# Kernel optimization log

Measured on AMD Instinct MI355X. Metric: run time of the kernel, lower is better.

The kernel has to match this reference:

```python
import jax, jax.numpy as jnp
import numpy as np

B, T, Rn, D, O, E, H, C, TM = 20, 20, 20, 4096, 16, 512, 8, 68, 1900


def l2norm(x, axis=-1, eps=1e-12):
    return x / jnp.maximum(jnp.linalg.norm(x, axis=axis, keepdims=True), eps)


def setup_inputs() -> dict:
    key = jax.random.key(0)
    ks = jax.random.split(key, 10)
    return {
        "features": jax.random.normal(ks[0], (B, T, Rn, D), jnp.float32),
        "labels": jax.random.randint(ks[1], (B, O), 0, C),
        "temporal_mem": jax.random.normal(ks[2], (TM, T, D), jnp.float32),
        "entity_W": jax.random.normal(ks[3], (C, E), jnp.float32) / np.float32(np.sqrt(C)),
        "entity_b": jnp.zeros((E,), jnp.float32),
        "Wq": jax.random.normal(ks[4], (E, E), jnp.float32) / np.float32(np.sqrt(E)),
        "Wk": jax.random.normal(ks[5], (D, E), jnp.float32) / np.float32(np.sqrt(D)),
        "Wv": jax.random.normal(ks[6], (D, E), jnp.float32) / np.float32(np.sqrt(D)),
        "Wo": jax.random.normal(ks[7], (E, E), jnp.float32) / np.float32(np.sqrt(E)),
        "obj_W1": jax.random.normal(ks[8], (D, E), jnp.float32) / np.float32(np.sqrt(D)),
        "obj_b1": jnp.zeros((E,), jnp.float32),
        "obj_W2": jax.random.normal(ks[9], (E, 1), jnp.float32) / np.float32(np.sqrt(E)),
        "obj_b2": jnp.zeros((1,), jnp.float32),
    }


def reference(features, labels, temporal_mem, entity_W, entity_b, Wq, Wk, Wv, Wo,
              obj_W1, obj_b1, obj_W2, obj_b2):
    beta = 0.5   # loss mixing weight (module's beta)
    qgce = 0.7   # generalized-CE exponent
    Dh = E // H
    # region features, L2-normalized (dataset_feat == 'CVPR' path)
    Rf = l2norm(features)                                   # [B,T,Rn,D]

    # ---- temporal memory-bank kNN retrieval ----
    R_max = l2norm(jnp.max(Rf, axis=2))                     # [B,T,D] max-pool over regions
    mem_max = l2norm(jnp.max(temporal_mem, axis=1))         # [TM,D] max-pool over frames
    sim = jnp.einsum('btd,md->btm', R_max, mem_max)         # [B,T,TM]
    idx = jnp.argmax(sim, axis=-1)                          # [B,T] nearest memory slot
    Rp = temporal_mem[idx]                                  # [B,T,T,D] gathered memory videos
    mem_feat = jnp.max(Rp, axis=2)                          # [B,T,D]

    # ---- entity (object-label) embedding: one-hot with class 0 zeroed ----
    onehot = jax.nn.one_hot(labels, C, dtype=features.dtype)
    onehot = onehot * (labels != 0)[..., None].astype(features.dtype)
    Qe = onehot @ entity_W + entity_b                       # [B,O,E]

    # ---- multi-head attention fusion over regions + retrieved memory ----
    kv = jnp.concatenate([Rf.reshape(B, T * Rn, D), mem_feat], axis=1)  # [B,N,D]
    q = (Qe @ Wq).reshape(B, O, H, Dh)
    k = (kv @ Wk).reshape(B, -1, H, Dh)
    v = (kv @ Wv).reshape(B, -1, H, Dh)
    scores = jnp.einsum('bohd,bnhd->bhon', q, k) / np.float32(np.sqrt(Dh))
    attn = jax.nn.softmax(scores, axis=-1)
    fused = jnp.einsum('bhon,bnhd->bohd', attn, v).reshape(B, O, E) @ Wo  # [B,O,E]

    # ---- top-k region objectness selection + generalized CE ----
    QR = jax.lax.stop_gradient(jnp.mean(scores, axis=1)[:, :, :T * Rn].reshape(B, O, T, Rn))
    hi = jnp.argmax(QR, axis=-1)                            # [B,O,T] top-1 region
    lo = jnp.argmin(QR, axis=-1)                            # [B,O,T] low region
    bidx = jnp.arange(B)[:, None, None]
    tidx = jnp.arange(T)[None, None, :]
    R_high = Rf[bidx, tidx, hi]                             # [B,O,T,D]
    R_low = Rf[bidx, tidx, lo]                              # [B,O,T,D]
    osel = (labels != 0).astype(features.dtype)             # [B,O]
    onum = jnp.maximum(jnp.sum(osel, axis=1), 1.0)
    mlp = lambda x: jax.nn.sigmoid(jnp.tanh(x @ obj_W1 + obj_b1) @ obj_W2 + obj_b2)
    s_hi = mlp(R_high * osel[..., None, None]).squeeze(-1)  # [B,O,T]
    s_lo = mlp(R_low * osel[..., None, None]).squeeze(-1)
    gce_hi = jnp.mean((1.0 - (s_hi + 1e-7) ** qgce) / qgce * osel[..., None], axis=-1)
    gce_lo = jnp.mean((1.0 - (1.0 - s_lo + 1e-7) ** qgce) / qgce * osel[..., None], axis=-1)
    gce = jnp.mean(jnp.sum(gce_hi, axis=1) / onum) + jnp.mean(jnp.sum(gce_lo, axis=1) / onum)

    return fused + beta * gce
```

## Files before the change

kernel.cpp:

```cpp
#include <hip/hip_runtime.h>

#define B_   20
#define T_   20
#define RN   20
#define D_   4096
#define O_   16
#define E_   512
#define H_   8
#define DH   64
#define TM_  1900
#define MREG 8192
#define NW   1536
#define NSIM 2048
#define MSIM 512
#define NG   1024
#define CAP  256
#define SIMK 8
#define GK   4

using f32x4  = __attribute__((ext_vector_type(4))) float;
using bf16x8 = __attribute__((ext_vector_type(8))) __bf16;

__device__ __forceinline__ unsigned short f2bf(float f){
  unsigned u = __float_as_uint(f);
  u += 0x7fffu + ((u >> 16) & 1u);
  return (unsigned short)(u >> 16);
}

__device__ __forceinline__ void st_bf4(unsigned short* dst, float4 v){
  ushort4 o = make_ushort4(f2bf(v.x), f2bf(v.y), f2bf(v.z), f2bf(v.w));
  *(ushort4*)dst = o;
}

__device__ __forceinline__ float bsum256(float v, float* sh){
  int t = threadIdx.x;
  for (int o = 32; o; o >>= 1) v += __shfl_down(v, o, 64);
  __syncthreads();
  if ((t & 63) == 0) sh[t >> 6] = v;
  __syncthreads();
  return sh[0] + sh[1] + sh[2] + sh[3];
}

__device__ __forceinline__ float bmax256(float v, float* sh){
  int t = threadIdx.x;
  for (int o = 32; o; o >>= 1) v = fmaxf(v, __shfl_down(v, o, 64));
  __syncthreads();
  if ((t & 63) == 0) sh[t >> 6] = v;
  __syncthreads();
  return fmaxf(fmaxf(sh[0], sh[1]), fmaxf(sh[2], sh[3]));
}

__device__ __forceinline__ void gld16(const void* g, void* l){
  __builtin_amdgcn_global_load_lds(
      (const __attribute__((address_space(1))) unsigned int*)g,
      (__attribute__((address_space(3))) unsigned int*)l, 16, 0, 0);
}

__global__ __launch_bounds__(256) void k_prelight(
    const float* __restrict__ F,
    const float* __restrict__ Wk, const float* __restrict__ Wv, const float* __restrict__ W1,
    unsigned short* __restrict__ Wall,
    unsigned short* __restrict__ A, float* __restrict__ rmaxr, float* __restrict__ rmsum,
    unsigned short* __restrict__ ubf,
    const int* __restrict__ labels, const float* __restrict__ entW, const float* __restrict__ entB,
    const float* __restrict__ Wq, float* __restrict__ q){
  __shared__ char smem[4352];
  int bid = blockIdx.x, t = threadIdx.x;
  if (bid < 512){
    int bt = bid;
    if (bt >= 400){
      int4 zz = make_int4(0,0,0,0);
      int4* r1 = (int4*)(ubf + (size_t)bt*D_);
      r1[t] = zz; r1[t + 256] = zz;
      int base = 8000 + (bt - 400)*2;
#pragma unroll
      for (int k = 0; k < 2; ++k){
        if (base + k < MREG){
          int4* r2 = (int4*)(A + (size_t)(base + k)*D_);
          r2[t] = zz; r2[t + 256] = zz;
        }
      }
      return;
    }
    float* sh = (float*)smem;
    const float* fb = F + (size_t)bt*RN*D_;
    unsigned short* ab = A + (size_t)bt*RN*D_;
    float4 mx[4];
#pragma unroll
    for (int i = 0; i < 4; ++i) mx[i] = make_float4(-1e30f,-1e30f,-1e30f,-1e30f);
    float4 vn[4];
#pragma unroll
    for (int i = 0; i < 4; ++i) vn[i] = *(const float4*)(fb + i*1024 + t*4);
    for (int r = 0; r < RN; ++r){
      float4 v[4];
      float s = 0.f;
#pragma unroll
      for (int i = 0; i < 4; ++i){
        v[i] = vn[i];
        s += v[i].x*v[i].x + v[i].y*v[i].y + v[i].z*v[i].z + v[i].w*v[i].w;
      }
      if (r + 1 < RN){
#pragma unroll
        for (int i = 0; i < 4; ++i)
          vn[i] = *(const float4*)(fb + (size_t)(r+1)*D_ + i*1024 + t*4);
      }
      s = bsum256(s, sh);
      float ri = 1.f / fmaxf(sqrtf(s), 1e-12f);
#pragma unroll
      for (int i = 0; i < 4; ++i){
        v[i].x *= ri; v[i].y *= ri; v[i].z *= ri; v[i].w *= ri;
        st_bf4(ab + (size_t)r*D_ + i*1024 + t*4, v[i]);
        mx[i].x = fmaxf(mx[i].x, v[i].x); mx[i].y = fmaxf(mx[i].y, v[i].y);
        mx[i].z = fmaxf(mx[i].z, v[i].z); mx[i].w = fmaxf(mx[i].w, v[i].w);
      }
    }
    float s2 = 0.f;
#pragma unroll
    for (int i = 0; i < 4; ++i){
      *(float4*)(rmaxr + (size_t)bt*D_ + i*1024 + t*4) = mx[i];
      s2 += mx[i].x*mx[i].x + mx[i].y*mx[i].y + mx[i].z*mx[i].z + mx[i].w*mx[i].w;
    }
    s2 = bsum256(s2, sh);
    if (t == 0) rmsum[bt] = s2;
    float inv = 1.f / fmaxf(sqrtf(s2), 1e-12f);
#pragma unroll
    for (int i = 0; i < 4; ++i){
      float4 u = mx[i];
      u.x *= inv; u.y *= inv; u.z *= inv; u.w *= inv;
      st_bf4(ubf + (size_t)bt*D_ + i*1024 + t*4, u);
    }
  } else if (bid < 6656){
    int wti = bid - 512;
    float* tile = (float*)smem;
    int kb = (wti & 127) * 32, nb = (wti >> 7) * 32;
    const float* src; int nc0;
    if (nb < 512)      { src = Wk; nc0 = nb; }
    else if (nb < 1024){ src = Wv; nc0 = nb - 512; }
    else               { src = W1; nc0 = nb - 1024; }
    int tx = t & 31, ty = t >> 5;
#pragma unroll
    for (int j = 0; j < 4; ++j){
      int k = kb + ty + j*8;
      tile[(ty + j*8)*33 + tx] = src[(size_t)k*E_ + nc0 + tx];
    }
    __syncthreads();
#pragma unroll
    for (int j = 0; j < 4; ++j){
      int n = nb + ty + j*8;
      int k = kb + tx;
      Wall[(size_t)n*D_ + k] = f2bf(tile[tx*33 + ty + j*8]);
    }
  } else {
    int bo = bid - 6656;
    float* qe = (float*)smem;
    int lab = labels[bo];
    float sel = (lab != 0) ? 1.f : 0.f;
    qe[t]       = sel * entW[(size_t)lab*E_ + t]       + entB[t];
    qe[t + 256] = sel * entW[(size_t)lab*E_ + t + 256] + entB[t + 256];
    __syncthreads();
    float a0 = 0.f, a1 = 0.f;
    for (int ep = 0; ep < E_; ++ep){
      float r = qe[ep];
      a0 += r * Wq[(size_t)ep*E_ + t];
      a1 += r * Wq[(size_t)ep*E_ + t + 256];
    }
    q[(size_t)bo*E_ + t] = a0;
    q[(size_t)bo*E_ + t + 256] = a1;
  }
}

__global__ __launch_bounds__(512, 1) void k_mix(
    const unsigned short* __restrict__ Akv, const unsigned short* __restrict__ Wall,
    float* __restrict__ C2,
    const float* __restrict__ TMm, float* __restrict__ umax, float* __restrict__ msum,
    unsigned short* __restrict__ gbf){
  __shared__ char lds[131072];
  int bid = blockIdx.x, t = threadIdx.x;
  if (bid < 192){
    int sb = (bid & 7)*24 + (bid >> 3);
    int mt = sb / 6, nt = sb % 6;
    int tid = t, wid = tid >> 6, l = tid & 63;
    int wr = (wid >> 2) * 128;
    int wc = (wid & 3) * 64;
    int fr = l & 15, fq = l >> 4;
    const char* Ab = (const char*)Akv + (size_t)mt*256*(size_t)(D_*2);
    const char* Bb = (const char*)Wall + (size_t)nt*256*(size_t)(D_*2);
    f32x4 acc[8][4];
#pragma unroll
    for (int m = 0; m < 8; ++m)
#pragma unroll
      for (int n = 0; n < 4; ++n) acc[m][n] = (f32x4){0.f,0.f,0.f,0.f};
#pragma unroll
    for (int i = 0; i < 4; ++i){
      int idx = i*512 + tid;
      int row = idx >> 3, u = idx & 7;
      int ul = u ^ (row & 7);
      gld16(Ab + (size_t)row*(D_*2) + (size_t)(ul*16), lds + idx*16);
      gld16(Bb + (size_t)row*(D_*2) + (size_t)(ul*16), lds + 32768 + idx*16);
    }
    __syncthreads();
    int c = 0;
    for (int kt = 0; kt < D_/64; ++kt){
      if (kt < D_/64 - 1){
        int ktoff = (kt + 1) * 128;
        char* dA = lds + (c^1)*65536;
        char* dB = dA + 32768;
#pragma unroll
        for (int i = 0; i < 4; ++i){
          int idx = i*512 + tid;
          int row = idx >> 3, u = idx & 7;
          int ul = u ^ (row & 7);
          gld16(Ab + (size_t)row*(D_*2) + ktoff + ul*16, dA + idx*16);
          gld16(Bb + (size_t)row*(D_*2) + ktoff + ul*16, dB + idx*16);
        }
      }
      const char* LA = lds + c*65536;
      const char* LB = LA + 32768;
      bf16x8 bv[4][2];
#pragma unroll
      for (int n = 0; n < 4; ++n)
#pragma unroll
        for (int kk = 0; kk < 2; ++kk){
          int row = wc + n*16 + fr;
          int u = (kk*4 + fq) ^ (row & 7);
          bv[n][kk] = *(const bf16x8*)(LB + row*128 + u*16);
        }
      __builtin_amdgcn_s_setprio(1);
#pragma unroll
      for (int mp = 0; mp < 4; ++mp){
        bf16x8 av[2][2];
#pragma unroll
        for (int mm = 0; mm < 2; ++mm)
#pragma unroll
          for (int kk = 0; kk < 2; ++kk){
            int row = wr + (mp*2 + mm)*16 + fr;
            int u = (kk*4 + fq) ^ (row & 7);
            av[mm][kk] = *(const bf16x8*)(LA + row*128 + u*16);
          }
#pragma unroll
        for (int mm = 0; mm < 2; ++mm)
#pragma unroll
          for (int n = 0; n < 4; ++n)
#pragma unroll
            for (int kk = 0; kk < 2; ++kk)
              acc[mp*2 + mm][n] = __builtin_amdgcn_mfma_f32_16x16x32_bf16(
                  av[mm][kk], bv[n][kk], acc[mp*2 + mm][n], 0, 0, 0);
      }
      __builtin_amdgcn_s_setprio(0);
      __syncthreads();
      c ^= 1;
    }
    size_t crow0 = (size_t)mt*256 + wr, ccol0 = (size_t)nt*256 + wc;
#pragma unroll
    for (int m = 0; m < 8; ++m)
#pragma unroll
      for (int n = 0; n < 4; ++n){
        size_t r0 = crow0 + m*16 + fq*4, c0 = ccol0 + n*16 + fr;
#pragma unroll
        for (int j = 0; j < 4; ++j)
          C2[(r0 + j)*(size_t)NW + c0] = acc[m][n][j];
      }
  } else {
    int m = bid - 192;
    if (m >= TM_){
      int4 zz = make_int4(0,0,0,0);
      ((int4*)(gbf + (size_t)m*D_))[t] = zz;
      return;
    }
    float* sh = (float*)lds;
    const float* base = TMm + (size_t)m*T_*D_;
    float4 mx[2];
#pragma unroll
    for (int i = 0; i < 2; ++i) mx[i] = make_float4(-1e30f,-1e30f,-1e30f,-1e30f);
    float4 va[2][2];
#pragma unroll
    for (int i = 0; i < 2; ++i) va[0][i] = *(const float4*)(base + i*2048 + t*4);
#pragma unroll
    for (int f = 0; f < T_; ++f){
      int c = f & 1;
      if (f + 1 < T_){
#pragma unroll
        for (int i = 0; i < 2; ++i)
          va[c^1][i] = *(const float4*)(base + (size_t)(f+1)*D_ + i*2048 + t*4);
      }
#pragma unroll
      for (int i = 0; i < 2; ++i){
        mx[i].x = fmaxf(mx[i].x, va[c][i].x); mx[i].y = fmaxf(mx[i].y, va[c][i].y);
        mx[i].z = fmaxf(mx[i].z, va[c][i].z); mx[i].w = fmaxf(mx[i].w, va[c][i].w);
      }
    }
    float s = 0.f;
#pragma unroll
    for (int i = 0; i < 2; ++i){
      *(float4*)(umax + (size_t)m*D_ + i*2048 + t*4) = mx[i];
      st_bf4(gbf + (size_t)m*D_ + i*2048 + t*4, mx[i]);
      s += mx[i].x*mx[i].x + mx[i].y*mx[i].y + mx[i].z*mx[i].z + mx[i].w*mx[i].w;
    }
    for (int o = 32; o; o >>= 1) s += __shfl_down(s, o, 64);
    __syncthreads();
    if ((t & 63) == 0) sh[t >> 6] = s;
    __syncthreads();
    if (t == 0){
      float tot = 0.f;
#pragma unroll
      for (int w = 0; w < 8; ++w) tot += sh[w];
      msum[m] = tot;
    }
  }
}

__global__ __launch_bounds__(512, 1) void k_simg(
    const unsigned short* __restrict__ ubf, const unsigned short* __restrict__ gbf,
    const unsigned short* __restrict__ Wall,
    float* __restrict__ simp, float* __restrict__ Gcp){
  __shared__ char lds[131072];
  int bid = blockIdx.x;
  bid = (bid & 7)*32 + (bid >> 3);
  const unsigned short *A, *Bw; float* C; int ldc, mt, nt, kt0, nkt;
  if (bid < 128){
    int p = bid >> 4, s = bid & 15;
    A = ubf; Bw = gbf; C = simp + (size_t)p*MSIM*NSIM; ldc = NSIM;
    mt = s >> 3; nt = s & 7; kt0 = p*(64/SIMK); nkt = 64/SIMK;
  } else {
    int s2 = bid - 128;
    int p = s2 >> 5, idx = s2 & 31;
    A = gbf; Bw = Wall; C = Gcp + (size_t)p*NSIM*NG; ldc = NG;
    mt = idx >> 2; nt = idx & 3; kt0 = p*(64/GK); nkt = 64/GK;
  }
  int tid = threadIdx.x, wid = tid >> 6, l = tid & 63;
  int wr = (wid >> 2) * 128;
  int wc = (wid & 3) * 64;
  int fr = l & 15, fq = l >> 4;
  const char* Ab = (const char*)A + (size_t)mt*256*(size_t)(D_*2);
  const char* Bb = (const char*)Bw + (size_t)nt*256*(size_t)(D_*2);
  f32x4 acc[8][4];
#pragma unroll
  for (int m = 0; m < 8; ++m)
#pragma unroll
    for (int n = 0; n < 4; ++n) acc[m][n] = (f32x4){0.f,0.f,0.f,0.f};
#pragma unroll
  for (int i = 0; i < 4; ++i){
    int idx = i*512 + tid;
    int row = idx >> 3, u = idx & 7;
    int ul = u ^ (row & 7);
    gld16(Ab + (size_t)row*(D_*2) + (size_t)(kt0*128 + ul*16), lds + idx*16);
    gld16(Bb + (size_t)row*(D_*2) + (size_t)(kt0*128 + ul*16), lds + 32768 + idx*16);
  }
  __syncthreads();
  int c = 0;
  for (int kt = kt0; kt < kt0 + nkt; ++kt){
    if (kt < kt0 + nkt - 1){
      int ktoff = (kt + 1) * 128;
      char* dA = lds + (c^1)*65536;
      char* dB = dA + 32768;
#pragma unroll
      for (int i = 0; i < 4; ++i){
        int idx = i*512 + tid;
        int row = idx >> 3, u = idx & 7;
        int ul = u ^ (row & 7);
        gld16(Ab + (size_t)row*(D_*2) + ktoff + ul*16, dA + idx*16);
        gld16(Bb + (size_t)row*(D_*2) + ktoff + ul*16, dB + idx*16);
      }
    }
    const char* LA = lds + c*65536;
    const char* LB = LA + 32768;
    bf16x8 bv[4][2];
#pragma unroll
    for (int n = 0; n < 4; ++n)
#pragma unroll
      for (int kk = 0; kk < 2; ++kk){
        int row = wc + n*16 + fr;
        int u = (kk*4 + fq) ^ (row & 7);
        bv[n][kk] = *(const bf16x8*)(LB + row*128 + u*16);
      }
    __builtin_amdgcn_s_setprio(1);
#pragma unroll
    for (int mp = 0; mp < 4; ++mp){
      bf16x8 av[2][2];
#pragma unroll
      for (int mm = 0; mm < 2; ++mm)
#pragma unroll
        for (int kk = 0; kk < 2; ++kk){
          int row = wr + (mp*2 + mm)*16 + fr;
          int u = (kk*4 + fq) ^ (row & 7);
          av[mm][kk] = *(const bf16x8*)(LA + row*128 + u*16);
        }
#pragma unroll
      for (int mm = 0; mm < 2; ++mm)
#pragma unroll
        for (int n = 0; n < 4; ++n)
#pragma unroll
          for (int kk = 0; kk < 2; ++kk)
            acc[mp*2 + mm][n] = __builtin_amdgcn_mfma_f32_16x16x32_bf16(
                av[mm][kk], bv[n][kk], acc[mp*2 + mm][n], 0, 0, 0);
    }
    __builtin_amdgcn_s_setprio(0);
    __syncthreads();
    c ^= 1;
  }
  size_t crow0 = (size_t)mt*256 + wr, ccol0 = (size_t)nt*256 + wc;
#pragma unroll
  for (int m = 0; m < 8; ++m)
#pragma unroll
    for (int n = 0; n < 4; ++n){
      size_t r0 = crow0 + m*16 + fq*4, c0 = ccol0 + n*16 + fr;
#pragma unroll
      for (int j = 0; j < 4; ++j)
        C[(r0 + j)*(size_t)ldc + c0] = acc[m][n][j];
    }
}

__global__ __launch_bounds__(256) void k_pick(const float* __restrict__ simp,
                                              const float* __restrict__ rmaxr, const float* __restrict__ rmsum,
                                              const float* __restrict__ umax, const float* __restrict__ msum,
                                              const float* __restrict__ Gcp, float* __restrict__ C2){
  int bt = blockIdx.x, t = threadIdx.x;
  __shared__ float srow[1920];
  __shared__ float sh[4];
  __shared__ int cnt;
  __shared__ int cl[CAP];
  for (int m = t; m < TM_; m += 256){
    float s = 0.f;
#pragma unroll
    for (int p = 0; p < SIMK; ++p)
      s += simp[(size_t)p*MSIM*NSIM + (size_t)bt*NSIM + m];
    srow[m] = s * (1.f / fmaxf(sqrtf(msum[m]), 1e-12f));
  }
  if (t == 0) cnt = 0;
  __syncthreads();
  float mx = -1e30f;
  for (int m = t; m < TM_; m += 256) mx = fmaxf(mx, srow[m]);
  mx = bmax256(mx, sh);
  float thr = mx - 2.5e-4f;
  for (int m = t; m < TM_; m += 256){
    if (srow[m] >= thr){
      int p = atomicAdd(&cnt, 1);
      if (p < CAP) cl[p] = m;
    }
  }
  __syncthreads();
  int cn = cnt < CAP ? cnt : CAP;
  float rinvv = 1.f / fmaxf(sqrtf(rmsum[bt]), 1e-12f);
  const float* a = rmaxr + (size_t)bt*D_;
  float best = -1e30f; int bestm = 0x7fffffff;
  for (int ci = 0; ci < cn; ++ci){
    int m = cl[ci];
    const float* wrow = umax + (size_t)m*D_;
    float p = 0.f;
    for (int i = t*4; i < D_; i += 1024){
      float4 av = *(const float4*)(a + i);
      float4 wv = *(const float4*)(wrow + i);
      p += av.x*wv.x + av.y*wv.y + av.z*wv.z + av.w*wv.w;
    }
    p = bsum256(p, sh);
    float sim = p * rinvv * (1.f / fmaxf(sqrtf(msum[m]), 1e-12f));
    if (sim > best || (sim == best && m < bestm)){ best = sim; bestm = m; }
  }
  float* dst = C2 + (size_t)(MREG + bt)*NW;
  int j = t*4;
  float4 accv = make_float4(0.f,0.f,0.f,0.f);
#pragma unroll
  for (int p = 0; p < GK; ++p){
    float4 v = *(const float4*)(Gcp + (size_t)p*NSIM*NG + (size_t)bestm*NG + j);
    accv.x += v.x; accv.y += v.y; accv.z += v.z; accv.w += v.w;
  }
  *(float4*)(dst + j) = accv;
}

__global__ __launch_bounds__(256) void k_post(const float* __restrict__ q, const float* __restrict__ c2,
                                              float* __restrict__ fpre, int* __restrict__ hi,
                                              int* __restrict__ lo, const float* __restrict__ b1,
                                              const float* __restrict__ W2, const float* __restrict__ b2,
                                              float* __restrict__ z){
  __shared__ char smem[58368];
  int bid = blockIdx.x, t = threadIdx.x;
  if (bid < 160){
    int b = bid >> 3, h = bid & 7;
    int w = t >> 6, l = t & 63;
    float* qhp = (float*)smem;
    float* kb  = (float*)(smem + 4160);
    float* sc  = (float*)(smem + 31460);
    for (int i = t; i < O_*DH; i += 256){
      int o = i >> 6, d = i & 63;
      qhp[o*65 + d] = q[((size_t)(b*O_ + o))*E_ + h*DH + d] * 0.125f;
    }
    __syncthreads();
    for (int c = 0; c < 4; ++c){
      for (int i = t; i < 105*DH; i += 256){
        int j = i >> 6, d = i & 63;
        int n = c*105 + j;
        size_t row = n < 400 ? (size_t)b*400 + n : (size_t)MREG + b*20 + (n - 400);
        kb[j*65 + d] = c2[row*NW + h*DH + d];
      }
      __syncthreads();
      for (int i = t; i < O_*105; i += 256){
        int o = i / 105, j = i % 105;
        float acc = 0.f;
        for (int d = 0; d < DH; ++d) acc += qhp[o*65 + d] * kb[j*65 + d];
        sc[o*420 + c*105 + j] = acc;
      }
      __syncthreads();
    }
    for (int oi = 0; oi < 4; ++oi){
      int o = w + oi*4;
      float mxv = -1e30f;
      for (int n = l; n < 420; n += 64) mxv = fmaxf(mxv, sc[o*420 + n]);
      for (int of = 32; of; of >>= 1) mxv = fmaxf(mxv, __shfl_xor(mxv, of, 64));
      float sum = 0.f;
      for (int n = l; n < 420; n += 64){ float e = expf(sc[o*420 + n] - mxv); sc[o*420 + n] = e; sum += e; }
      for (int of = 32; of; of >>= 1) sum += __shfl_xor(sum, of, 64);
      float inv = 1.f / sum;
      for (int n = l; n < 420; n += 64) sc[o*420 + n] *= inv;
    }
    __syncthreads();
    float acc[4] = {0.f, 0.f, 0.f, 0.f};
    for (int c = 0; c < 4; ++c){
      for (int i = t; i < 105*DH; i += 256){
        int j = i >> 6, d = i & 63;
        int n = c*105 + j;
        size_t row = n < 400 ? (size_t)b*400 + n : (size_t)MREG + b*20 + (n - 400);
        kb[j*65 + d] = c2[row*NW + E_ + h*DH + d];
      }
      __syncthreads();
#pragma unroll
      for (int og = 0; og < 4; ++og){
        int o = og*4 + w;
        float a = 0.f;
        for (int j = 0; j < 105; ++j) a += sc[o*420 + c*105 + j] * kb[j*65 + l];
        acc[og] += a;
      }
      __syncthreads();
    }
#pragma unroll
    for (int og = 0; og < 4; ++og){
      int o = og*4 + w;
      fpre[((size_t)(b*O_ + o))*E_ + h*DH + l] = acc[og];
    }
  } else if (bid < 560){
    int bt = bid - 160;
    int b = bt / T_, tt = bt % T_;
    float* kl = (float*)smem;
    float* qr = (float*)(smem + 41040);
    for (int i = t; i < RN*E_; i += 256){
      int r = i >> 9, e = i & 511;
      kl[r*513 + e] = c2[((size_t)b*400 + tt*RN + r)*NW + e];
    }
    __syncthreads();
#pragma unroll
    for (int pp = 0; pp < 2; ++pp){
      int p = t + pp*256;
      if (p < O_*RN){
        int o = p / RN, r = p % RN;
        const float* qrow = q + ((size_t)(b*O_ + o))*E_;
        float acc = 0.f;
        for (int e = 0; e < E_; ++e) acc += qrow[e] * kl[r*513 + e];
        qr[o*20 + r] = acc;
      }
    }
    __syncthreads();
    if (t < O_){
      int o = t;
      float bh = qr[o*20], bl = qr[o*20]; int ih = 0, il = 0;
#pragma unroll
      for (int r = 1; r < RN; ++r){
        float v = qr[o*20 + r];
        if (v > bh){ bh = v; ih = r; }
        if (v < bl){ bl = v; il = r; }
      }
      int rowbase = b*400 + tt*RN;
      int outi = (b*O_ + o)*T_ + tt;
      hi[outi] = rowbase + ih;
      lo[outi] = rowbase + il;
    }
  } else {
    int g = (bid - 560)*4 + (t >> 6);
    int l = t & 63;
    const float* hrow = c2 + (size_t)g*NW + 1024;
    float acc = 0.f;
    for (int e = l; e < E_; e += 64) acc += tanhf(hrow[e] + b1[e]) * W2[e];
    for (int of = 32; of; of >>= 1) acc += __shfl_down(acc, of, 64);
    if (l == 0) z[g] = 1.f / (1.f + expf(-(acc + b2[0])));
  }
}

__global__ __launch_bounds__(256) void k_outg(const float* __restrict__ fpre, const float* __restrict__ Wo,
                                              const float* __restrict__ z, const int* __restrict__ hi,
                                              const int* __restrict__ lo, const int* __restrict__ labels,
                                              float* __restrict__ out){
  int bo = blockIdx.x, t = threadIdx.x;
  __shared__ float rowv[E_];
  __shared__ float vb[B_];
  __shared__ int cb[B_];
  __shared__ float gsh;
  rowv[t] = fpre[(size_t)bo*E_ + t];
  rowv[t + 256] = fpre[(size_t)bo*E_ + t + 256];
  if (t < B_){ vb[t] = 0.f; cb[t] = 0; }
  __syncthreads();
  for (int p = t; p < B_*O_; p += 256){
    int b = p / O_;
    if (labels[p] != 0){
      float acc = 0.f;
      for (int tt = 0; tt < T_; ++tt){
        float shi = z[hi[p*T_ + tt]];
        float slo = z[lo[p*T_ + tt]];
        acc += (1.f - __powf(shi + 1e-7f, 0.7f)) / 0.7f;
        acc += (1.f - __powf(1.f - slo + 1e-7f, 0.7f)) / 0.7f;
      }
      atomicAdd(&vb[b], acc / (float)T_);
      atomicAdd(&cb[b], 1);
    }
  }
  __syncthreads();
  if (t == 0){
    float g = 0.f;
    for (int b = 0; b < B_; ++b) g += vb[b] / fmaxf((float)cb[b], 1.f);
    gsh = 0.5f * (g / (float)B_);
  }
  __syncthreads();
  float g = gsh;
  float a0 = 0.f, a1 = 0.f;
  for (int ep = 0; ep < E_; ++ep){
    float r = rowv[ep];
    a0 += r * Wo[(size_t)ep*E_ + t];
    a1 += r * Wo[(size_t)ep*E_ + t + 256];
  }
  out[(size_t)bo*E_ + t] = a0 + g;
  out[(size_t)bo*E_ + t + 256] = a1 + g;
}

extern "C" void kernel_launch(void* const* d_in, const int* in_sizes, int n_in,
                              void* d_out, int out_size, void* d_ws, size_t ws_size,
                              hipStream_t stream) {
  (void)in_sizes; (void)n_in; (void)out_size; (void)ws_size;
  const float* F    = (const float*)d_in[0];
  const int*   labels = (const int*)d_in[1];
  const float* TMm  = (const float*)d_in[2];
  const float* entW = (const float*)d_in[3];
  const float* entB = (const float*)d_in[4];
  const float* Wq   = (const float*)d_in[5];
  const float* Wk   = (const float*)d_in[6];
  const float* Wv   = (const float*)d_in[7];
  const float* Wo   = (const float*)d_in[8];
  const float* W1   = (const float*)d_in[9];
  const float* b1   = (const float*)d_in[10];
  const float* W2   = (const float*)d_in[11];
  const float* b2   = (const float*)d_in[12];
  float* out = (float*)d_out;

  size_t off = 0;
  char* wsb = (char*)d_ws;
  auto alloc = [&](size_t bytes) -> char* {
    char* p = wsb + off; off += (bytes + 255) & ~(size_t)255; return p;
  };
  unsigned short* A_kv = (unsigned short*)alloc((size_t)MREG * D_ * 2);
  unsigned short* Wall = (unsigned short*)alloc((size_t)NW * D_ * 2);
  float* umax          = (float*)alloc((size_t)TM_ * D_ * 4);
  unsigned short* gbf  = (unsigned short*)alloc((size_t)NSIM * D_ * 2);
  unsigned short* ubf  = (unsigned short*)alloc((size_t)MSIM * D_ * 2);
  float* rmaxr = (float*)alloc((size_t)400 * D_ * 4);
  float* simp  = (float*)alloc((size_t)SIMK * MSIM * NSIM * 4);
  float* Gcp   = (float*)alloc((size_t)GK * NSIM * NG * 4);
  float* C2    = (float*)alloc((size_t)(MREG + 512) * NW * 4);
  float* qbuf  = (float*)alloc((size_t)B_ * O_ * E_ * 4);
  float* fpre  = (float*)alloc((size_t)B_ * O_ * E_ * 4);
  float* rmsum = (float*)alloc(400 * 4);
  float* msum  = (float*)alloc(TM_ * 4);
  int*   hib   = (int*)alloc(6400 * 4);
  int*   lob   = (int*)alloc(6400 * 4);
  float* zbuf  = (float*)alloc(8000 * 4);

  k_prelight<<<6976, 256, 0, stream>>>(F, Wk, Wv, W1, Wall, A_kv, rmaxr, rmsum, ubf,
                                       labels, entW, entB, Wq, qbuf);
  k_mix<<<2240, 512, 0, stream>>>(A_kv, Wall, C2, TMm, umax, msum, gbf);
  k_simg<<<256, 512, 0, stream>>>(ubf, gbf, Wall, simp, Gcp);
  k_pick<<<400, 256, 0, stream>>>(simp, rmaxr, rmsum, umax, msum, Gcp, C2);
  k_post<<<2560, 256, 0, stream>>>(qbuf, C2, fpre, hib, lob, b1, W2, b2, zbuf);
  k_outg<<<B_*O_, 256, 0, stream>>>(fpre, Wo, zbuf, hib, lob, labels, out);
}
```

Baseline: 494.3 us.

## Split k_mix GEMM along K into two partial buffers and interleave with memory-max blocks

The big bf16 GEMM in k_mix is split in two along the K dimension, so 384 tiles each run half the K loop and write to separate partial output buffers C2p0 and C2p1. The consumers in k_post now add the two partials when they read. Block indices are regrouped so each group of 19 blocks holds 3 GEMM blocks and 16 temporal-memory max blocks, spreading the heavy GEMM work evenly across the grid instead of front-loading 192 long blocks. This adds an extra 8192x1536 fp32 buffer write and read and extra loads in k_post, in exchange for better load balance and more GEMM parallelism.

```diff
diff --git a/kernel.cpp b/kernel.cpp
--- a/kernel.cpp
+++ b/kernel.cpp
@@ -171,14 +171,18 @@
 
 __global__ __launch_bounds__(512, 1) void k_mix(
     const unsigned short* __restrict__ Akv, const unsigned short* __restrict__ Wall,
-    float* __restrict__ C2,
+    float* __restrict__ C2p0, float* __restrict__ C2p1,
     const float* __restrict__ TMm, float* __restrict__ umax, float* __restrict__ msum,
     unsigned short* __restrict__ gbf){
   __shared__ char lds[131072];
-  int bid = blockIdx.x, t = threadIdx.x;
-  if (bid < 192){
-    int sb = (bid & 7)*24 + (bid >> 3);
-    int mt = sb / 6, nt = sb % 6;
+  int g = blockIdx.x / 19, r = blockIdx.x % 19;
+  int t = threadIdx.x;
+  if (r < 3){
+    int mi = g*3 + r;
+    int p = mi & 1, tile = mi >> 1;
+    int mt = tile / 6, nt = tile % 6;
+    int kt0 = p * 32;
+    float* C = p ? C2p1 : C2p0;
     int tid = t, wid = tid >> 6, l = tid & 63;
     int wr = (wid >> 2) * 128;
     int wc = (wid & 3) * 64;
@@ -195,13 +199,13 @@
       int idx = i*512 + tid;
       int row = idx >> 3, u = idx & 7;
       int ul = u ^ (row & 7);
-      gld16(Ab + (size_t)row*(D_*2) + (size_t)(ul*16), lds + idx*16);
-      gld16(Bb + (size_t)row*(D_*2) + (size_t)(ul*16), lds + 32768 + idx*16);
+      gld16(Ab + (size_t)row*(D_*2) + (size_t)(kt0*128 + ul*16), lds + idx*16);
+      gld16(Bb + (size_t)row*(D_*2) + (size_t)(kt0*128 + ul*16), lds + 32768 + idx*16);
     }
     __syncthreads();
     int c = 0;
-    for (int kt = 0; kt < D_/64; ++kt){
-      if (kt < D_/64 - 1){
+    for (int kt = kt0; kt < kt0 + 32; ++kt){
+      if (kt < kt0 + 31){
         int ktoff = (kt + 1) * 128;
         char* dA = lds + (c^1)*65536;
         char* dB = dA + 32768;
@@ -258,10 +262,10 @@
         size_t r0 = crow0 + m*16 + fq*4, c0 = ccol0 + n*16 + fr;
 #pragma unroll
         for (int j = 0; j < 4; ++j)
-          C2[(r0 + j)*(size_t)NW + c0] = acc[m][n][j];
+          C[(r0 + j)*(size_t)NW + c0] = acc[m][n][j];
       }
   } else {
-    int m = bid - 192;
+    int m = g*16 + (r - 3);
     if (m >= TM_){
       int4 zz = make_int4(0,0,0,0);
       ((int4*)(gbf + (size_t)m*D_))[t] = zz;
@@ -413,7 +417,7 @@
 __global__ __launch_bounds__(256) void k_pick(const float* __restrict__ simp,
                                               const float* __restrict__ rmaxr, const float* __restrict__ rmsum,
                                               const float* __restrict__ umax, const float* __restrict__ msum,
-                                              const float* __restrict__ Gcp, float* __restrict__ C2){
+                                              const float* __restrict__ Gcp, float* __restrict__ C2p0){
   int bt = blockIdx.x, t = threadIdx.x;
   __shared__ float srow[1920];
   __shared__ float sh[4];
@@ -456,7 +460,7 @@
     float sim = p * rinvv * (1.f / fmaxf(sqrtf(msum[m]), 1e-12f));
     if (sim > best || (sim == best && m < bestm)){ best = sim; bestm = m; }
   }
-  float* dst = C2 + (size_t)(MREG + bt)*NW;
+  float* dst = C2p0 + (size_t)(MREG + bt)*NW;
   int j = t*4;
   float4 accv = make_float4(0.f,0.f,0.f,0.f);
 #pragma unroll
@@ -467,7 +471,8 @@
   *(float4*)(dst + j) = accv;
 }
 
-__global__ __launch_bounds__(256) void k_post(const float* __restrict__ q, const float* __restrict__ c2,
+__global__ __launch_bounds__(256) void k_post(const float* __restrict__ q,
+                                              const float* __restrict__ c2a, const float* __restrict__ c2b,
                                               float* __restrict__ fpre, int* __restrict__ hi,
                                               int* __restrict__ lo, const float* __restrict__ b1,
                                               const float* __restrict__ W2, const float* __restrict__ b2,
@@ -489,8 +494,14 @@
       for (int i = t; i < 105*DH; i += 256){
         int j = i >> 6, d = i & 63;
         int n = c*105 + j;
-        size_t row = n < 400 ? (size_t)b*400 + n : (size_t)MREG + b*20 + (n - 400);
-        kb[j*65 + d] = c2[row*NW + h*DH + d];
+        float kv;
+        if (n < 400){
+          size_t ro = ((size_t)b*400 + n)*NW + h*DH + d;
+          kv = c2a[ro] + c2b[ro];
+        } else {
+          kv = c2a[((size_t)MREG + b*20 + (n - 400))*NW + h*DH + d];
+        }
+        kb[j*65 + d] = kv;
       }
       __syncthreads();
       for (int i = t; i < O_*105; i += 256){
@@ -518,8 +529,14 @@
       for (int i = t; i < 105*DH; i += 256){
         int j = i >> 6, d = i & 63;
         int n = c*105 + j;
-        size_t row = n < 400 ? (size_t)b*400 + n : (size_t)MREG + b*20 + (n - 400);
-        kb[j*65 + d] = c2[row*NW + E_ + h*DH + d];
+        float vv;
+        if (n < 400){
+          size_t ro = ((size_t)b*400 + n)*NW + E_ + h*DH + d;
+          vv = c2a[ro] + c2b[ro];
+        } else {
+          vv = c2a[((size_t)MREG + b*20 + (n - 400))*NW + E_ + h*DH + d];
+        }
+        kb[j*65 + d] = vv;
       }
       __syncthreads();
 #pragma unroll
@@ -543,7 +560,8 @@
     float* qr = (float*)(smem + 41040);
     for (int i = t; i < RN*E_; i += 256){
       int r = i >> 9, e = i & 511;
-      kl[r*513 + e] = c2[((size_t)b*400 + tt*RN + r)*NW + e];
+      size_t ro = ((size_t)b*400 + tt*RN + r)*NW + e;
+      kl[r*513 + e] = c2a[ro] + c2b[ro];
     }
     __syncthreads();
 #pragma unroll
@@ -575,9 +593,10 @@
   } else {
     int g = (bid - 560)*4 + (t >> 6);
     int l = t & 63;
-    const float* hrow = c2 + (size_t)g*NW + 1024;
+    const float* h0 = c2a + (size_t)g*NW + 1024;
+    const float* h1 = c2b + (size_t)g*NW + 1024;
     float acc = 0.f;
-    for (int e = l; e < E_; e += 64) acc += tanhf(hrow[e] + b1[e]) * W2[e];
+    for (int e = l; e < E_; e += 64) acc += tanhf(h0[e] + h1[e] + b1[e]) * W2[e];
     for (int of = 32; of; of >>= 1) acc += __shfl_down(acc, of, 64);
     if (l == 0) z[g] = 1.f / (1.f + expf(-(acc + b2[0])));
   }
@@ -660,7 +679,8 @@
   float* rmaxr = (float*)alloc((size_t)400 * D_ * 4);
   float* simp  = (float*)alloc((size_t)SIMK * MSIM * NSIM * 4);
   float* Gcp   = (float*)alloc((size_t)GK * NSIM * NG * 4);
-  float* C2    = (float*)alloc((size_t)(MREG + 512) * NW * 4);
+  float* C2p0  = (float*)alloc((size_t)(MREG + 512) * NW * 4);
+  float* C2p1  = (float*)alloc((size_t)MREG * NW * 4);
   float* qbuf  = (float*)alloc((size_t)B_ * O_ * E_ * 4);
   float* fpre  = (float*)alloc((size_t)B_ * O_ * E_ * 4);
   float* rmsum = (float*)alloc(400 * 4);
@@ -671,9 +691,9 @@
 
   k_prelight<<<6976, 256, 0, stream>>>(F, Wk, Wv, W1, Wall, A_kv, rmaxr, rmsum, ubf,
                                        labels, entW, entB, Wq, qbuf);
-  k_mix<<<2240, 512, 0, stream>>>(A_kv, Wall, C2, TMm, umax, msum, gbf);
+  k_mix<<<2432, 512, 0, stream>>>(A_kv, Wall, C2p0, C2p1, TMm, umax, msum, gbf);
   k_simg<<<256, 512, 0, stream>>>(ubf, gbf, Wall, simp, Gcp);
-  k_pick<<<400, 256, 0, stream>>>(simp, rmaxr, rmsum, umax, msum, Gcp, C2);
-  k_post<<<2560, 256, 0, stream>>>(qbuf, C2, fpre, hib, lob, b1, W2, b2, zbuf);
+  k_pick<<<400, 256, 0, stream>>>(simp, rmaxr, rmsum, umax, msum, Gcp, C2p0);
+  k_post<<<2560, 256, 0, stream>>>(qbuf, C2p0, C2p1, fpre, hib, lob, b1, W2, b2, zbuf);
   k_outg<<<B_*O_, 256, 0, stream>>>(fpre, Wo, zbuf, hib, lob, labels, out);
 }
```

Result: slower. 570.8 us (+15.5%).
